# Performance work log

Hardware: AMD Instinct MI355X
Metric: run time of the kernel (lower is better)

## Reference

```python
import jax, jax.numpy as jnp
import numpy as np

B, T, N, I = 64, 12, 307, 3   # batch, timesteps, nodes, input features
R, D = 64, 10                 # rnn_units, embed_dim


def setup_inputs() -> dict:
    key = jax.random.key(0)
    ks = iter(jax.random.split(key, 64))
    def p(*shape):
        return jax.random.normal(next(ks), shape, jnp.float32) * 0.1
    return dict(
        x=jax.random.normal(next(ks), (B, T, N, I), jnp.float32),
        node_emb1=p(N, D), node_emb2=p(N, D),
        # x_embedding MLP: 1 -> 16 -> 2 -> D
        xe_w1=p(16, 1), xe_b1=p(16), xe_w2=p(2, 16), xe_b2=p(2), xe_w3=p(D, 2), xe_b3=p(D),
        # fc1 MLP: I -> 16 -> 2 -> D
        fc1_w1=p(16, I), fc1_b1=p(16), fc1_w2=p(2, 16), fc1_b2=p(2), fc1_w3=p(D, 2), fc1_b3=p(D),
        # fc2 MLP: R -> 16 -> 2 -> D
        fc2_w1=p(16, R), fc2_b1=p(16), fc2_w2=p(2, 16), fc2_b2=p(2), fc2_w3=p(D, 2), fc2_b3=p(D),
        # GRU1 (input D -> hidden R), gates ordered r,z,n as in torch
        gru1_wih=p(3 * R, D), gru1_whh=p(3 * R, R), gru1_bih=p(3 * R), gru1_bhh=p(3 * R),
        # GRU2 (input R -> hidden R)
        gru2_wih=p(3 * R, R), gru2_whh=p(3 * R, R), gru2_bih=p(3 * R), gru2_bhh=p(3 * R),
        weights_pool=p(D, R, R), bias_pool=p(D, R),
        # 1x1 conv == linear over channels: [R, 2R]
        diff_w=p(R, 2 * R), diff_b=p(R),
    )


def _mlp(x, w1, b1, w2, b2, w3, b3):
    h = jax.nn.sigmoid(x @ w1.T + b1)
    h = jax.nn.sigmoid(h @ w2.T + b2)
    return h @ w3.T + b3


def _gru(xs, h0, wih, whh, bih, bhh):
    # xs: [T, B', Din]; torch GRU gate order: r, z, n
    xw = xs @ wih.T + bih  # precompute input projections [T, B', 3R]
    def step(h, xw_t):
        hw = h @ whh.T + bhh
        xr, xz, xn = jnp.split(xw_t, 3, -1)
        hr, hz, hn = jnp.split(hw, 3, -1)
        r = jax.nn.sigmoid(xr + hr)
        z = jax.nn.sigmoid(xz + hz)
        n = jnp.tanh(xn + r * hn)
        h = (1.0 - z) * n + z * h
        return h, h
    _, out = jax.lax.scan(step, h0, xw)
    return out  # [T, B', R]


def reference(x, node_emb1, node_emb2,
              xe_w1, xe_b1, xe_w2, xe_b2, xe_w3, xe_b3,
              fc1_w1, fc1_b1, fc1_w2, fc1_b2, fc1_w3, fc1_b3,
              fc2_w1, fc2_b1, fc2_w2, fc2_b2, fc2_w3, fc2_b3,
              gru1_wih, gru1_whh, gru1_bih, gru1_bhh,
              gru2_wih, gru2_whh, gru2_bih, gru2_bhh,
              weights_pool, bias_pool, diff_w, diff_b):
    # --- feature-level dynamic dependency ---
    node_embed = _mlp(x[..., None], xe_w1, xe_b1, xe_w2, xe_b2, xe_w3, xe_b3)  # [B,T,N,I,D]
    supports_node2 = jax.nn.relu(jnp.einsum('btnjd,btnid->btnji', node_embed, node_embed))  # [B,T,N,I,I]
    # x1 = eye(I) @ x == x (identity support kept implicit)
    x2 = jnp.einsum('btnji,btni->btnj', supports_node2, x)
    input_for_fc1 = x + x2
    g1_in = _mlp(input_for_fc1, fc1_w1, fc1_b1, fc1_w2, fc1_b2, fc1_w3, fc1_b3)  # [B,T,N,D]
    g1_in = jnp.transpose(g1_in, (1, 0, 2, 3)).reshape(T, B * N, D)
    h0 = jnp.zeros((B * N, R), jnp.float32)
    out1 = _gru(g1_in, h0, gru1_wih, gru1_whh, gru1_bih, gru1_bhh).reshape(T, B, N, R)
    # --- node-level dynamic dependency ---
    filt = _mlp(out1, fc2_w1, fc2_b1, fc2_w2, fc2_b2, fc2_w3, fc2_b3)  # [T,B,N,D]
    nodevec = jnp.tanh(node_emb1 * filt)  # broadcast [N,D] over [T,B,N,D]
    supports2 = jax.nn.relu(jnp.einsum('tbnd,tbmd->tbnm', nodevec, nodevec))  # [T,B,N,N]
    # x_g1 = eye(N) @ out1 == out1
    x_g = out1 + jnp.einsum('tbnm,tbmc->tbnc', supports2, out1)
    weights = jnp.einsum('nd,dcr->ncr', node_emb2, weights_pool)  # [N,R,R]
    bias = node_emb2 @ bias_pool                                   # [N,R]
    diff1 = jnp.einsum('tbnc,ncr->tbnr', x_g, weights) + bias      # [T,B,N,R]
    # --- 1x1 conv over channels + GRU2 (dropout in eval mode: identity) ---
    cat = jnp.concatenate([out1, diff1], axis=-1)                  # [T,B,N,2R]
    g2_in = jnp.einsum('tbnc,rc->tbnr', cat, diff_w) + diff_b      # [T,B,N,R]
    out2 = _gru(g2_in.reshape(T, B * N, R), h0, gru2_wih, gru2_whh, gru2_bih, gru2_bhh)
    return jnp.transpose(out2.reshape(T, B, N, R), (1, 0, 2, 3))   # [B,T,N,R]
```

## Files before the change

kernel.cpp:

```cpp
#include <hip/hip_runtime.h>
#include <hip/hip_fp16.h>
#include <math.h>

#define B_ 64
#define T_ 12
#define N_ 307
#define I_ 3
#define R_ 64
#define D_ 10
#define M_ (B_*N_)
#define TM_ (T_*M_)

typedef _Float16 f16x8 __attribute__((ext_vector_type(8)));
typedef float f32x4 __attribute__((ext_vector_type(4)));

__device__ __forceinline__ float sigm(float x){ return 1.f/(1.f+__expf(-x)); }

__device__ __forceinline__ unsigned pkh(float a, float b){
  unsigned r;
  asm("v_cvt_pkrtz_f16_f32 %0, %1, %2" : "=v"(r) : "v"(a), "v"(b));
  return r;
}

__global__ __launch_bounds__(256) void k_stageA(
    const float* __restrict__ x,
    const float* __restrict__ xw1, const float* __restrict__ xb1,
    const float* __restrict__ xw2, const float* __restrict__ xb2,
    const float* __restrict__ xw3, const float* __restrict__ xb3,
    const float* __restrict__ fw1, const float* __restrict__ fb1,
    const float* __restrict__ fw2, const float* __restrict__ fb2,
    const float* __restrict__ fw3, const float* __restrict__ fb3,
    float* __restrict__ g1)
{
  int idx = blockIdx.x*256 + threadIdx.x;
  int t = idx / M_;
  int m = idx - t*M_;
  int b = m / N_;
  int n = m - b*N_;
  const float* xp = x + (((size_t)b*T_ + t)*N_ + n)*I_;
  float xv[3] = {xp[0], xp[1], xp[2]};
  float e[3][10];
  #pragma unroll
  for (int i=0;i<3;++i){
    float h1[16];
    #pragma unroll
    for (int u=0;u<16;++u) h1[u] = sigm(xv[i]*xw1[u] + xb1[u]);
    float h2[2];
    #pragma unroll
    for (int v=0;v<2;++v){
      float a = xb2[v];
      #pragma unroll
      for (int u=0;u<16;++u) a += h1[u]*xw2[v*16+u];
      h2[v] = sigm(a);
    }
    #pragma unroll
    for (int d=0;d<10;++d) e[i][d] = xb3[d] + h2[0]*xw3[d*2] + h2[1]*xw3[d*2+1];
  }
  float in1[3];
  #pragma unroll
  for (int j=0;j<3;++j){
    float acc = 0.f;
    #pragma unroll
    for (int i=0;i<3;++i){
      float s = 0.f;
      #pragma unroll
      for (int d=0;d<10;++d) s += e[j][d]*e[i][d];
      s = fmaxf(s, 0.f);
      acc += s*xv[i];
    }
    in1[j] = xv[j] + acc;
  }
  float h1[16];
  #pragma unroll
  for (int u=0;u<16;++u)
    h1[u] = sigm(fb1[u] + in1[0]*fw1[u*3] + in1[1]*fw1[u*3+1] + in1[2]*fw1[u*3+2]);
  float h2[2];
  #pragma unroll
  for (int v=0;v<2;++v){
    float a = fb2[v];
    #pragma unroll
    for (int u=0;u<16;++u) a += h1[u]*fw2[v*16+u];
    h2[v] = sigm(a);
  }
  float* gp = g1 + (size_t)idx*10;
  #pragma unroll
  for (int d=0;d<10;++d) gp[d] = fb3[d] + h2[0]*fw3[d*2] + h2[1]*fw3[d*2+1];
}

__global__ __launch_bounds__(256) void k_wn(
    const float* __restrict__ emb2, const float* __restrict__ wpool,
    const float* __restrict__ bpool, float* __restrict__ Wn, float* __restrict__ bn)
{
  int n = blockIdx.x; int tid = threadIdx.x;
  __shared__ float e_s[10];
  if (tid < 10) e_s[tid] = emb2[n*10 + tid];
  __syncthreads();
  #pragma unroll
  for (int e=0;e<16;++e){
    int i = e*256 + tid;
    float a = 0.f;
    #pragma unroll
    for (int d=0;d<10;++d) a += e_s[d]*wpool[(size_t)d*4096 + i];
    Wn[(size_t)n*4096 + i] = a;
  }
  if (tid < 64){
    float a = 0.f;
    #pragma unroll
    for (int d=0;d<10;++d) a += e_s[d]*bpool[d*64 + tid];
    bn[n*64 + tid] = a;
  }
}

__global__ __launch_bounds__(256) void k_wf(
    const float* __restrict__ Wn, const float* __restrict__ bn,
    const float* __restrict__ dw, const float* __restrict__ db,
    float* __restrict__ Wf, float* __restrict__ bf)
{
  int n = blockIdx.x; int tid = threadIdx.x;
  __shared__ float WnS[64*68];
  __shared__ float dwBT[64*68];
  __shared__ float bn_s[64];
  for (int idx = tid; idx < 4096; idx += 256) {
    int c = idx >> 6, r = idx & 63;
    WnS[c*68 + r] = Wn[(size_t)n*4096 + idx];
  }
  for (int idx = tid; idx < 4096; idx += 256) {
    int u = idx >> 6, r = idx & 63;
    dwBT[r*68 + u] = dw[u*128 + 64 + r];
  }
  if (tid < 64) bn_s[tid] = bn[n*64 + tid];
  __syncthreads();
  int u = tid & 63, cg = tid >> 6;
  #pragma unroll
  for (int j = 0; j < 16; ++j) {
    int c = cg*16 + j;
    float acc = 0.f;
    #pragma unroll 8
    for (int r = 0; r < 64; ++r) acc += WnS[c*68 + r] * dwBT[r*68 + u];
    Wf[(size_t)n*4096 + u*64 + c] = acc;
  }
  if (tid < 64) {
    float acc = db[tid];
    #pragma unroll 8
    for (int r = 0; r < 64; ++r) acc += bn_s[r] * dwBT[r*68 + tid];
    bf[n*64 + tid] = acc;
  }
}

__global__ __launch_bounds__(256) void k_wpackM(
    const float* __restrict__ wih2, const float* __restrict__ whh2,
    const float* __restrict__ wih1, const float* __restrict__ whh1,
    unsigned* __restrict__ Wh2, unsigned* __restrict__ Wx2,
    unsigned* __restrict__ Wh1, unsigned* __restrict__ Wx1)
{
  int i = blockIdx.x*256 + threadIdx.x;
  if (i < 192*32) {
    int wr = i >> 5, p = i & 31;
    Wh2[i] = pkh(whh2[wr*64 + 2*p], whh2[wr*64 + 2*p + 1]);
    Wx2[i] = pkh(wih2[wr*64 + 2*p], wih2[wr*64 + 2*p + 1]);
    Wh1[i] = pkh(whh1[wr*64 + 2*p], whh1[wr*64 + 2*p + 1]);
  }
  int j = i - 192*32;
  if (j >= 0 && j < 192*16) {
    int wr = j >> 4, p = j & 15;
    Wx1[j] = (p < 5) ? pkh(wih1[wr*10 + 2*p], wih1[wr*10 + 2*p + 1]) : 0u;
  }
}

template<int DIN, bool WFIN>
__global__ __launch_bounds__(256, 3) void k_gruM(
    const float* __restrict__ xseq,
    const unsigned* __restrict__ Whf,
    const unsigned* __restrict__ Wxf,
    const float* __restrict__ bih, const float* __restrict__ bhh,
    float* __restrict__ o_out)
{
  constexpr int XPR = (DIN == 64) ? 32 : 16;
  constexpr int XKS = XPR / 16;
  constexpr int XST = XPR + 4;
  __shared__ __align__(16) unsigned Ah_s[16*36];
  __shared__ __align__(16) unsigned Ax_s[16*XST];
  const int tid = threadIdx.x;
  const int lane = tid & 63, w = tid >> 6;
  const int fr = lane & 15, fq = lane >> 4;
  const int row0 = blockIdx.x * 16;
  const int u = w*16 + fr;

  f16x8 bh_r[2], bh_z[2], bh_n[2];
  #pragma unroll
  for (int ks = 0; ks < 2; ++ks) {
    bh_r[ks] = *(const f16x8*)&Whf[(size_t)u*32        + ks*16 + fq*4];
    bh_z[ks] = *(const f16x8*)&Whf[(size_t)(64+u)*32   + ks*16 + fq*4];
    bh_n[ks] = *(const f16x8*)&Whf[(size_t)(128+u)*32  + ks*16 + fq*4];
  }
  f16x8 bx_r[XKS], bx_z[XKS], bx_n[XKS];
  #pragma unroll
  for (int ks = 0; ks < XKS; ++ks) {
    bx_r[ks] = *(const f16x8*)&Wxf[(size_t)u*XPR       + ks*16 + fq*4];
    bx_z[ks] = *(const f16x8*)&Wxf[(size_t)(64+u)*XPR  + ks*16 + fq*4];
    bx_n[ks] = *(const f16x8*)&Wxf[(size_t)(128+u)*XPR + ks*16 + fq*4];
  }

  const float brc = bih[u]     + bhh[u];
  const float bzc = bih[64+u]  + bhh[64+u];
  const float bxn = bih[128+u];
  const float bhn = bhh[128+u];

  for (int i = tid; i < 16*36;  i += 256) Ah_s[i] = 0u;
  for (int i = tid; i < 16*XST; i += 256) Ax_s[i] = 0u;
  __syncthreads();

  size_t obase[4];
  #pragma unroll
  for (int reg = 0; reg < 4; ++reg) {
    int g = row0 + fq*4 + reg;
    if (WFIN) { int bb = g / N_, nn = g - bb*N_; obase[reg] = (((size_t)bb*T_)*N_ + nn)*64 + u; }
    else      { obase[reg] = (size_t)g*64 + u; }
  }
  const size_t tstep = WFIN ? (size_t)N_*64 : (size_t)M_*64;
  float hreg[4] = {0.f, 0.f, 0.f, 0.f};

  for (int t = 0; t < T_; ++t) {
    if (DIN == 64) {
      #pragma unroll
      for (int it = 0; it < 2; ++it) {
        int idx = tid + it*256;
        int row = idx >> 5, p = idx & 31;
        const float2 v = *(const float2*)&xseq[((size_t)t*M_ + row0 + row)*64 + 2*p];
        Ax_s[row*XST + p] = pkh(v.x, v.y);
      }
    } else {
      if (tid < 80) {
        int row = tid / 5, p = tid - (tid/5)*5;
        const float2 v = *(const float2*)&xseq[((size_t)t*M_ + row0 + row)*10 + 2*p];
        Ax_s[row*XST + p] = pkh(v.x, v.y);
      }
    }
    __syncthreads();

    f32x4 ar  = {0.f,0.f,0.f,0.f}, az  = {0.f,0.f,0.f,0.f};
    f32x4 anh = {0.f,0.f,0.f,0.f}, anx = {0.f,0.f,0.f,0.f};
    #pragma unroll
    for (int ks = 0; ks < 2; ++ks) {
      f16x8 ah = *(const f16x8*)&Ah_s[fr*36 + ks*16 + fq*4];
      ar  = __builtin_amdgcn_mfma_f32_16x16x32_f16(ah, bh_r[ks], ar,  0,0,0);
      az  = __builtin_amdgcn_mfma_f32_16x16x32_f16(ah, bh_z[ks], az,  0,0,0);
      anh = __builtin_amdgcn_mfma_f32_16x16x32_f16(ah, bh_n[ks], anh, 0,0,0);
    }
    #pragma unroll
    for (int ks = 0; ks < XKS; ++ks) {
      f16x8 ax = *(const f16x8*)&Ax_s[fr*XST + ks*16 + fq*4];
      ar  = __builtin_amdgcn_mfma_f32_16x16x32_f16(ax, bx_r[ks], ar,  0,0,0);
      az  = __builtin_amdgcn_mfma_f32_16x16x32_f16(ax, bx_z[ks], az,  0,0,0);
      anx = __builtin_amdgcn_mfma_f32_16x16x32_f16(ax, bx_n[ks], anx, 0,0,0);
    }

    float o_new[4];
    #pragma unroll
    for (int reg = 0; reg < 4; ++reg) {
      float rg = sigm(ar[reg] + brc);
      float zg = sigm(az[reg] + bzc);
      float ng = tanhf(anx[reg] + bxn + rg*(anh[reg] + bhn));
      o_new[reg] = (1.f - zg)*ng + zg*hreg[reg];
      hreg[reg] = o_new[reg];
    }
    #pragma unroll
    for (int reg = 0; reg < 4; ++reg)
      o_out[obase[reg] + (size_t)t*tstep] = o_new[reg];

    unsigned pk[4];
    #pragma unroll
    for (int reg = 0; reg < 4; ++reg) {
      float pr = __shfl_xor(o_new[reg], 1);
      pk[reg] = pkh(o_new[reg], pr);
    }
    __syncthreads();
    if ((fr & 1) == 0) {
      #pragma unroll
      for (int reg = 0; reg < 4; ++reg)
        Ah_s[(fq*4 + reg)*36 + w*8 + (fr >> 1)] = pk[reg];
    }
  }
}

__global__ __launch_bounds__(256) void k_stageC(
    const float* __restrict__ out1, const float* __restrict__ emb1,
    const float* __restrict__ w1, const float* __restrict__ b1,
    const float* __restrict__ w2, const float* __restrict__ b2,
    const float* __restrict__ w3, const float* __restrict__ b3,
    float* __restrict__ ndv)
{
  int idx = blockIdx.x*256 + threadIdx.x;
  int m = idx % M_;
  int n = m % N_;
  float rv[64];
  const float4* r4 = (const float4*)(out1 + (size_t)idx*64);
  #pragma unroll
  for (int q=0;q<16;++q){ float4 v=r4[q]; rv[q*4]=v.x; rv[q*4+1]=v.y; rv[q*4+2]=v.z; rv[q*4+3]=v.w; }
  float h1[16];
  for (int u=0;u<16;++u){
    float a = b1[u];
    const float* wr = w1 + u*64;
    #pragma unroll
    for (int c=0;c<64;++c) a += rv[c]*wr[c];
    h1[u] = sigm(a);
  }
  float h2[2];
  #pragma unroll
  for (int v=0;v<2;++v){
    float a = b2[v];
    #pragma unroll
    for (int u=0;u<16;++u) a += h1[u]*w2[v*16+u];
    h2[v] = sigm(a);
  }
  #pragma unroll
  for (int d=0;d<10;++d){
    float f = b3[d] + h2[0]*w3[d*2] + h2[1]*w3[d*2+1];
    ndv[(size_t)idx*10 + d] = tanhf(emb1[n*10+d]*f);
  }
}

__global__ __launch_bounds__(256, 2) void k_stageDM(
    const float* __restrict__ ndv, const float* __restrict__ out1, float* __restrict__ xg)
{
  int tb = blockIdx.x;
  const int tid = threadIdx.x;
  const int lane = tid & 63, wid = tid >> 6;
  const int fr = lane & 15, fq = lane >> 4;

  __shared__ __align__(16) unsigned Vp_s[320*20];
  __shared__ __align__(16) unsigned P_s[320*36];
  __shared__ __align__(16) unsigned O_s[64*36];

  for (int i = tid; i < 320*20; i += 256) {
    int nn = i / 20, p = i - nn*20;
    float a = 0.f, b = 0.f;
    if (nn < N_ && p < 5) {
      const float2 v = *(const float2*)&ndv[((size_t)tb*N_ + nn)*10 + 2*p];
      a = v.x; b = v.y;
    }
    Vp_s[i] = pkh(a, b);
  }
  __syncthreads();

  f32x4 acc[5][4];
  #pragma unroll
  for (int a = 0; a < 5; ++a)
    #pragma unroll
    for (int c = 0; c < 4; ++c)
      acc[a][c] = (f32x4){0.f, 0.f, 0.f, 0.f};

  const float* ob = out1 + (size_t)tb*N_*64;

  for (int mc = 0; mc < 320; mc += 64) {
    for (int it = tid; it < 512; it += 256) {
      int p = it >> 4, cg = it & 15;
      int m0 = mc + 2*p;
      float4 a = make_float4(0.f,0.f,0.f,0.f), b = a;
      if (m0     < N_) a = *(const float4*)&ob[(size_t)m0*64 + cg*4];
      if (m0 + 1 < N_) b = *(const float4*)&ob[(size_t)(m0+1)*64 + cg*4];
      int c0 = cg*4;
      O_s[(c0+0)*36 + p] = pkh(a.x, b.x);
      O_s[(c0+1)*36 + p] = pkh(a.y, b.y);
      O_s[(c0+2)*36 + p] = pkh(a.z, b.z);
      O_s[(c0+3)*36 + p] = pkh(a.w, b.w);
    }
    {
      f16x8 va[4];
      #pragma unroll
      for (int mt = 0; mt < 4; ++mt)
        va[mt] = *(const f16x8*)&Vp_s[(mc + mt*16 + fr)*20 + fq*4];
      #pragma unroll
      for (int j = 0; j < 5; ++j) {
        int nt = wid + 4*j;
        f16x8 vb = *(const f16x8*)&Vp_s[(nt*16 + fr)*20 + fq*4];
        int nn = nt*16 + fr;
        #pragma unroll
        for (int mt = 0; mt < 4; ++mt) {
          f32x4 s = (f32x4){0.f,0.f,0.f,0.f};
          s = __builtin_amdgcn_mfma_f32_16x16x32_f16(va[mt], vb, s, 0, 0, 0);
          unsigned p0 = pkh(fmaxf(s[0],0.f), fmaxf(s[1],0.f));
          unsigned p1 = pkh(fmaxf(s[2],0.f), fmaxf(s[3],0.f));
          *(uint2*)&P_s[nn*36 + mt*8 + fq*2] = make_uint2(p0, p1);
        }
      }
    }
    __syncthreads();

    #pragma unroll
    for (int ks = 0; ks < 2; ++ks) {
      int kd = ks*16 + fq*4;
      f16x8 bf[4];
      #pragma unroll
      for (int ct = 0; ct < 4; ++ct)
        bf[ct] = *(const f16x8*)&O_s[(ct*16 + fr)*36 + kd];
      #pragma unroll
      for (int a = 0; a < 5; ++a) {
        f16x8 af = *(const f16x8*)&P_s[((wid + 4*a)*16 + fr)*36 + kd];
        #pragma unroll
        for (int ct = 0; ct < 4; ++ct)
          acc[a][ct] = __builtin_amdgcn_mfma_f32_16x16x32_f16(af, bf[ct], acc[a][ct], 0, 0, 0);
      }
    }
    __syncthreads();
  }

  #pragma unroll
  for (int a = 0; a < 5; ++a) {
    #pragma unroll
    for (int ct = 0; ct < 4; ++ct) {
      int col = ct*16 + fr;
      #pragma unroll
      for (int reg = 0; reg < 4; ++reg) {
        int n = (wid + 4*a)*16 + fq*4 + reg;
        if (n < N_) {
          size_t base = (size_t)tb*N_*64 + (size_t)n*64 + col;
          xg[base] = out1[base] + acc[a][ct][reg];
        }
      }
    }
  }
}

__global__ __launch_bounds__(256) void k_stageEM(
    const float* xg_in, const float* __restrict__ out1,
    const float* __restrict__ Wf, const float* __restrict__ dw,
    const float* __restrict__ bf,
    float* xg_out)
{
  int n = blockIdx.y;
  int tile = blockIdx.x;
  const int tid = threadIdx.x;
  const int lane = tid & 63, w = tid >> 6;
  const int fr = lane & 15, fq = lane >> 4;
  __shared__ __align__(16) unsigned As[64*68];
  __shared__ __align__(16) unsigned Bs[64*68];
  __shared__ float bf_s[64];

  for (int idx = tid; idx < 1024; idx += 256) {
    int row = idx >> 4, c4 = idx & 15;
    size_t g = ((size_t)(tile*64 + row)*N_ + n)*64 + c4*4;
    float4 o  = *(const float4*)&out1[g];
    float4 xv = *(const float4*)&xg_in[g];
    As[row*68 + c4*2]          = pkh(o.x, o.y);
    As[row*68 + c4*2 + 1]      = pkh(o.z, o.w);
    As[row*68 + 32 + c4*2]     = pkh(xv.x, xv.y);
    As[row*68 + 32 + c4*2 + 1] = pkh(xv.z, xv.w);
    int u = row;
    float4 da = *(const float4*)&dw[u*128 + c4*4];
    float4 wf = *(const float4*)&Wf[(size_t)n*4096 + u*64 + c4*4];
    Bs[u*68 + c4*2]          = pkh(da.x, da.y);
    Bs[u*68 + c4*2 + 1]      = pkh(da.z, da.w);
    Bs[u*68 + 32 + c4*2]     = pkh(wf.x, wf.y);
    Bs[u*68 + 32 + c4*2 + 1] = pkh(wf.z, wf.w);
  }
  if (tid < 64) bf_s[tid] = bf[n*64 + tid];
  __syncthreads();

  f32x4 acc[4];
  #pragma unroll
  for (int ct = 0; ct < 4; ++ct) acc[ct] = (f32x4){0.f,0.f,0.f,0.f};

  #pragma unroll
  for (int ks = 0; ks < 4; ++ks) {
    f16x8 af = *(const f16x8*)&As[(w*16 + fr)*68 + ks*16 + fq*4];
    #pragma unroll
    for (int ct = 0; ct < 4; ++ct) {
      f16x8 bfr = *(const f16x8*)&Bs[(ct*16 + fr)*68 + ks*16 + fq*4];
      acc[ct] = __builtin_amdgcn_mfma_f32_16x16x32_f16(af, bfr, acc[ct], 0, 0, 0);
    }
  }

  #pragma unroll
  for (int ct = 0; ct < 4; ++ct) {
    int u = ct*16 + fr;
    float bfv = bf_s[u];
    #pragma unroll
    for (int reg = 0; reg < 4; ++reg) {
      int row = w*16 + fq*4 + reg;
      xg_out[((size_t)(tile*64 + row)*N_ + n)*64 + u] = acc[ct][reg] + bfv;
    }
  }
}

extern "C" void kernel_launch(void* const* d_in, const int* in_sizes, int n_in,
                              void* d_out, int out_size, void* d_ws, size_t ws_size,
                              hipStream_t stream)
{
  (void)in_sizes; (void)n_in; (void)out_size;
  const float* x    = (const float*)d_in[0];
  const float* emb1 = (const float*)d_in[1];
  const float* emb2 = (const float*)d_in[2];
  const float* xw1  = (const float*)d_in[3];
  const float* xb1  = (const float*)d_in[4];
  const float* xw2  = (const float*)d_in[5];
  const float* xb2  = (const float*)d_in[6];
  const float* xw3  = (const float*)d_in[7];
  const float* xb3  = (const float*)d_in[8];
  const float* fw1  = (const float*)d_in[9];
  const float* fb1  = (const float*)d_in[10];
  const float* fw2  = (const float*)d_in[11];
  const float* fb2  = (const float*)d_in[12];
  const float* fw3  = (const float*)d_in[13];
  const float* fb3  = (const float*)d_in[14];
  const float* c2w1 = (const float*)d_in[15];
  const float* c2b1 = (const float*)d_in[16];
  const float* c2w2 = (const float*)d_in[17];
  const float* c2b2 = (const float*)d_in[18];
  const float* c2w3 = (const float*)d_in[19];
  const float* c2b3 = (const float*)d_in[20];
  const float* g1wih= (const float*)d_in[21];
  const float* g1whh= (const float*)d_in[22];
  const float* g1bih= (const float*)d_in[23];
  const float* g1bhh= (const float*)d_in[24];
  const float* g2wih= (const float*)d_in[25];
  const float* g2whh= (const float*)d_in[26];
  const float* g2bih= (const float*)d_in[27];
  const float* g2bhh= (const float*)d_in[28];
  const float* wpool= (const float*)d_in[29];
  const float* bpool= (const float*)d_in[30];
  const float* dww  = (const float*)d_in[31];
  const float* dwb  = (const float*)d_in[32];
  float* out = (float*)d_out;

  float* ws = (float*)d_ws;
  float* g1_in = ws;
  float* out1  = g1_in + (size_t)TM_*10;
  float* ndv   = out1 + (size_t)TM_*64;
  float* xg    = ndv + (size_t)TM_*10;
  float* Wn    = xg + (size_t)TM_*64;
  float* bn    = Wn + (size_t)N_*4096;
  float* Wf    = bn + (size_t)N_*64;
  float* bf    = Wf + (size_t)N_*4096;
  unsigned* Wh2f = (unsigned*)(bf + (size_t)N_*64);
  unsigned* Wx2f = Wh2f + 192*32;
  unsigned* Wh1f = Wx2f + 192*32;
  unsigned* Wx1f = Wh1f + 192*32;
  size_t need = ((size_t)((char*)(Wx1f + 192*16) - (char*)ws));
  if (ws_size < need) return;

  k_stageA<<<TM_/256, 256, 0, stream>>>(x, xw1,xb1,xw2,xb2,xw3,xb3, fw1,fb1,fw2,fb2,fw3,fb3, g1_in);
  k_wn<<<N_, 256, 0, stream>>>(emb2, wpool, bpool, Wn, bn);
  k_wf<<<N_, 256, 0, stream>>>(Wn, bn, dww, dwb, Wf, bf);
  k_wpackM<<<(192*32 + 192*16 + 255)/256, 256, 0, stream>>>(
      g2wih, g2whh, g1wih, g1whh, Wh2f, Wx2f, Wh1f, Wx1f);

  k_gruM<10,false><<<M_/16, 256, 0, stream>>>(g1_in, Wh1f, Wx1f, g1bih, g1bhh, out1);

  k_stageC<<<TM_/256, 256, 0, stream>>>(out1, emb1, c2w1,c2b1,c2w2,c2b2,c2w3,c2b3, ndv);
  k_stageDM<<<T_*B_, 256, 0, stream>>>(ndv, out1, xg);
  k_stageEM<<<dim3(12, N_), 256, 0, stream>>>(xg, out1, Wf, dww, bf, xg);

  k_gruM<64,true><<<M_/16, 256, 0, stream>>>(xg, Wh2f, Wx2f, g2bih, g2bhh, out);
}
```

Before: 258.9 us.

## Split graph-conv kernel over 64-row node tiles and double-buffer out1 chunks

The node-similarity/aggregation kernel now launches five blocks per (t,b) pair, each owning a 64-row slice of output nodes instead of all 320. This cuts per-block accumulators and shared memory, which allows a higher occupancy bound. The out1 chunk staging is double-buffered so the next chunk's loads overlap the current MFMA work. In exchange, each block redundantly loads the full node-vector matrix and every out1 chunk, so global and LDS traffic rises roughly five-fold.

```diff
diff --git a/kernel.cpp b/kernel.cpp
--- a/kernel.cpp
+++ b/kernel.cpp
@@ -320,20 +320,22 @@
   }
 }
 
-__global__ __launch_bounds__(256, 2) void k_stageDM(
+__global__ __launch_bounds__(256, 3) void k_stageDM(
     const float* __restrict__ ndv, const float* __restrict__ out1, float* __restrict__ xg)
 {
-  int tb = blockIdx.x;
+  const int tile = blockIdx.x;
+  const int tb = blockIdx.y;
   const int tid = threadIdx.x;
   const int lane = tid & 63, wid = tid >> 6;
   const int fr = lane & 15, fq = lane >> 4;
+  const int nb0 = tile*64;
 
   __shared__ __align__(16) unsigned Vp_s[320*20];
-  __shared__ __align__(16) unsigned P_s[320*36];
-  __shared__ __align__(16) unsigned O_s[64*36];
+  __shared__ __align__(16) unsigned P_s[64*36];
+  __shared__ __align__(16) unsigned O_s[2][64*36];
 
   for (int i = tid; i < 320*20; i += 256) {
-    int nn = i / 20, p = i - nn*20;
+    int nn = i / 20, p = i - (i/20)*20;
     float a = 0.f, b = 0.f;
     if (nn < N_ && p < 5) {
       const float2 v = *(const float2*)&ndv[((size_t)tb*N_ + nn)*10 + 2*p];
@@ -341,82 +343,78 @@
     }
     Vp_s[i] = pkh(a, b);
   }
+
+  const float* ob = out1 + (size_t)tb*N_*64;
+
+  for (int it = tid; it < 512; it += 256) {
+    int p = it & 31, cg = it >> 5;
+    int m0 = 2*p;
+    float4 a = make_float4(0.f,0.f,0.f,0.f), b = a;
+    if (m0     < N_) a = *(const float4*)&ob[(size_t)m0*64 + cg*4];
+    if (m0 + 1 < N_) b = *(const float4*)&ob[(size_t)(m0+1)*64 + cg*4];
+    int c0 = cg*4;
+    O_s[0][(c0+0)*36 + p] = pkh(a.x, b.x);
+    O_s[0][(c0+1)*36 + p] = pkh(a.y, b.y);
+    O_s[0][(c0+2)*36 + p] = pkh(a.z, b.z);
+    O_s[0][(c0+3)*36 + p] = pkh(a.w, b.w);
+  }
   __syncthreads();
 
-  f32x4 acc[5][4];
-  #pragma unroll
-  for (int a = 0; a < 5; ++a)
-    #pragma unroll
-    for (int c = 0; c < 4; ++c)
-      acc[a][c] = (f32x4){0.f, 0.f, 0.f, 0.f};
-
-  const float* ob = out1 + (size_t)tb*N_*64;
-
-  for (int mc = 0; mc < 320; mc += 64) {
-    for (int it = tid; it < 512; it += 256) {
-      int p = it >> 4, cg = it & 15;
-      int m0 = mc + 2*p;
-      float4 a = make_float4(0.f,0.f,0.f,0.f), b = a;
-      if (m0     < N_) a = *(const float4*)&ob[(size_t)m0*64 + cg*4];
-      if (m0 + 1 < N_) b = *(const float4*)&ob[(size_t)(m0+1)*64 + cg*4];
-      int c0 = cg*4;
-      O_s[(c0+0)*36 + p] = pkh(a.x, b.x);
-      O_s[(c0+1)*36 + p] = pkh(a.y, b.y);
-      O_s[(c0+2)*36 + p] = pkh(a.z, b.z);
-      O_s[(c0+3)*36 + p] = pkh(a.w, b.w);
-    }
-    {
-      f16x8 va[4];
-      #pragma unroll
-      for (int mt = 0; mt < 4; ++mt)
-        va[mt] = *(const f16x8*)&Vp_s[(mc + mt*16 + fr)*20 + fq*4];
-      #pragma unroll
-      for (int j = 0; j < 5; ++j) {
-        int nt = wid + 4*j;
-        f16x8 vb = *(const f16x8*)&Vp_s[(nt*16 + fr)*20 + fq*4];
-        int nn = nt*16 + fr;
-        #pragma unroll
-        for (int mt = 0; mt < 4; ++mt) {
-          f32x4 s = (f32x4){0.f,0.f,0.f,0.f};
-          s = __builtin_amdgcn_mfma_f32_16x16x32_f16(va[mt], vb, s, 0, 0, 0);
-          unsigned p0 = pkh(fmaxf(s[0],0.f), fmaxf(s[1],0.f));
-          unsigned p1 = pkh(fmaxf(s[2],0.f), fmaxf(s[3],0.f));
-          *(uint2*)&P_s[nn*36 + mt*8 + fq*2] = make_uint2(p0, p1);
-        }
+  f16x8 vb = *(const f16x8*)&Vp_s[(nb0 + wid*16 + fr)*20 + fq*4];
+
+  f32x4 acc[4];
+  #pragma unroll
+  for (int ct = 0; ct < 4; ++ct) acc[ct] = (f32x4){0.f,0.f,0.f,0.f};
+
+  for (int k = 0; k < 5; ++k) {
+    const int cur = k & 1;
+    const int mc = k*64;
+    if (k < 4) {
+      int mcn = mc + 64;
+      for (int it = tid; it < 512; it += 256) {
+        int p = it & 31, cg = it >> 5;
+        int m0 = mcn + 2*p;
+        float4 a = make_float4(0.f,0.f,0.f,0.f), b = a;
+        if (m0     < N_) a = *(const float4*)&ob[(size_t)m0*64 + cg*4];
+        if (m0 + 1 < N_) b = *(const float4*)&ob[(size_t)(m0+1)*64 + cg*4];
+        int c0 = cg*4;
+        O_s[cur^1][(c0+0)*36 + p] = pkh(a.x, b.x);
+        O_s[cur^1][(c0+1)*36 + p] = pkh(a.y, b.y);
+        O_s[cur^1][(c0+2)*36 + p] = pkh(a.z, b.z);
+        O_s[cur^1][(c0+3)*36 + p] = pkh(a.w, b.w);
       }
     }
-    __syncthreads();
-
+    #pragma unroll
+    for (int mt = 0; mt < 4; ++mt) {
+      f16x8 va = *(const f16x8*)&Vp_s[(mc + mt*16 + fr)*20 + fq*4];
+      f32x4 s = (f32x4){0.f,0.f,0.f,0.f};
+      s = __builtin_amdgcn_mfma_f32_16x16x32_f16(va, vb, s, 0, 0, 0);
+      unsigned p0 = pkh(fmaxf(s[0],0.f), fmaxf(s[1],0.f));
+      unsigned p1 = pkh(fmaxf(s[2],0.f), fmaxf(s[3],0.f));
+      *(uint2*)&P_s[(wid*16 + fr)*36 + mt*8 + fq*2] = make_uint2(p0, p1);
+    }
     #pragma unroll
     for (int ks = 0; ks < 2; ++ks) {
       int kd = ks*16 + fq*4;
-      f16x8 bf[4];
+      f16x8 af = *(const f16x8*)&P_s[(wid*16 + fr)*36 + kd];
       #pragma unroll
-      for (int ct = 0; ct < 4; ++ct)
-        bf[ct] = *(const f16x8*)&O_s[(ct*16 + fr)*36 + kd];
-      #pragma unroll
-      for (int a = 0; a < 5; ++a) {
-        f16x8 af = *(const f16x8*)&P_s[((wid + 4*a)*16 + fr)*36 + kd];
-        #pragma unroll
-        for (int ct = 0; ct < 4; ++ct)
-          acc[a][ct] = __builtin_amdgcn_mfma_f32_16x16x32_f16(af, bf[ct], acc[a][ct], 0, 0, 0);
+      for (int ct = 0; ct < 4; ++ct) {
+        f16x8 bf = *(const f16x8*)&O_s[cur][(ct*16 + fr)*36 + kd];
+        acc[ct] = __builtin_amdgcn_mfma_f32_16x16x32_f16(af, bf, acc[ct], 0, 0, 0);
       }
     }
     __syncthreads();
   }
 
   #pragma unroll
-  for (int a = 0; a < 5; ++a) {
-    #pragma unroll
-    for (int ct = 0; ct < 4; ++ct) {
-      int col = ct*16 + fr;
-      #pragma unroll
-      for (int reg = 0; reg < 4; ++reg) {
-        int n = (wid + 4*a)*16 + fq*4 + reg;
-        if (n < N_) {
-          size_t base = (size_t)tb*N_*64 + (size_t)n*64 + col;
-          xg[base] = out1[base] + acc[a][ct][reg];
-        }
+  for (int ct = 0; ct < 4; ++ct) {
+    int col = ct*16 + fr;
+    #pragma unroll
+    for (int reg = 0; reg < 4; ++reg) {
+      int n = nb0 + wid*16 + fq*4 + reg;
+      if (n < N_) {
+        size_t base = (size_t)tb*N_*64 + (size_t)n*64 + col;
+        xg[base] = out1[base] + acc[ct][reg];
       }
     }
   }
@@ -548,7 +546,7 @@
   k_gruM<10,false><<<M_/16, 256, 0, stream>>>(g1_in, Wh1f, Wx1f, g1bih, g1bhh, out1);
 
   k_stageC<<<TM_/256, 256, 0, stream>>>(out1, emb1, c2w1,c2b1,c2w2,c2b2,c2w3,c2b3, ndv);
-  k_stageDM<<<T_*B_, 256, 0, stream>>>(ndv, out1, xg);
+  k_stageDM<<<dim3(5, T_*B_), 256, 0, stream>>>(ndv, out1, xg);
   k_stageEM<<<dim3(12, N_), 256, 0, stream>>>(xg, out1, Wf, dww, bf, xg);
 
   k_gruM<64,true><<<M_/16, 256, 0, stream>>>(xg, Wh2f, Wx2f, g2bih, g2bhh, out);
```

After: 290.7 us. +12.3%, slower.
